# Performance work log

Hardware: AMD Instinct MI355X
Metric: run time of the kernel (lower is better)

The kernel has to match this reference:

```python
import jax, jax.numpy as jnp
import numpy as np

B, S, D, H = 64, 2048, 64, 128  # batch, seq_len, input_dim, rnn_hidden_dim


def setup_inputs() -> dict:
    key = jax.random.key(0)
    k = jax.random.split(key, 6)
    x = jax.random.normal(k[0], (B, S, D), dtype=jnp.float32)
    # LSTM params, keras gate order: i, f, g(candidate), o
    Wx = jax.random.normal(k[1], (D, 4 * H), dtype=jnp.float32) / np.sqrt(D)
    Wh = jax.random.normal(k[2], (H, 4 * H), dtype=jnp.float32) / np.sqrt(H)
    b = jnp.zeros((4 * H,), dtype=jnp.float32).at[H:2 * H].set(1.0)  # unit_forget_bias
    # Dense(1, sigmoid) head
    Wd = jax.random.normal(k[3], (H, 1), dtype=jnp.float32) / np.sqrt(H)
    bd = jnp.zeros((1,), dtype=jnp.float32)
    return {"x": x, "Wx": Wx, "Wh": Wh, "b": b, "Wd": Wd, "bd": bd}


def _lstm_seq(x, Wx, Wh, b):
    H_ = Wh.shape[0]
    # precompute input projections for all timesteps: [B,S,4H]
    xz = jnp.einsum('bsd,dg->bsg', x, Wx) + b

    def step(carry, xz_t):
        h, c = carry
        z = xz_t + h @ Wh  # [B,4H]
        i = jax.nn.sigmoid(z[:, :H_])
        f = jax.nn.sigmoid(z[:, H_:2 * H_])
        g = jnp.tanh(z[:, 2 * H_:3 * H_])
        o = jax.nn.sigmoid(z[:, 3 * H_:])
        c = f * c + i * g
        h = o * jnp.tanh(c)
        return (h, c), h

    h0 = jnp.zeros((x.shape[0], H_), dtype=x.dtype)
    c0 = jnp.zeros((x.shape[0], H_), dtype=x.dtype)
    _, hs = jax.lax.scan(step, (h0, c0), jnp.swapaxes(xz, 0, 1))  # hs: [S,B,H]
    return jnp.swapaxes(hs, 0, 1)  # [B,S,H]


def reference(x, Wx, Wh, b, Wd, bd):
    h = _lstm_seq(x, Wx, Wh, b)                 # [B,S,H]
    return jax.nn.sigmoid(h @ Wd + bd)          # [B,S,1]
```

## Files before the change

kernel.cpp:

```cpp
#include <hip/hip_runtime.h>

#define B_ 64
#define S_ 2048
#define D_ 64
#define H_ 128
#define G_ 512
#define CH 16

typedef float f32x4 __attribute__((ext_vector_type(4)));
typedef short bf16x8 __attribute__((ext_vector_type(8)));

#define MFMA16(a, b, c) __builtin_amdgcn_mfma_f32_16x16x32_bf16((a), (b), (c), 0, 0, 0)
#define RCPF(x) __builtin_amdgcn_rcpf(x)
#define LOG2E 1.442695041f

#if __has_builtin(__builtin_amdgcn_exp2f)
#define EXP2(x) __builtin_amdgcn_exp2f(x)
#else
#define EXP2(x) exp2f(x)
#endif

#define STEP_SYNC() do {                                  \
    asm volatile("s_waitcnt lgkmcnt(0)" ::: "memory");    \
    __builtin_amdgcn_s_barrier();                         \
    asm volatile("" ::: "memory");                        \
} while (0)

__device__ __forceinline__ short f2bf(float f) {
    unsigned u = __builtin_bit_cast(unsigned, f);
    return (short)((u + 0x7FFFu + ((u >> 16) & 1u)) >> 16);
}
__device__ __forceinline__ float bflo(unsigned u) { return __builtin_bit_cast(float, u << 16); }
__device__ __forceinline__ float bfhi(unsigned u) { return __builtin_bit_cast(float, u & 0xFFFF0000u); }
__device__ __forceinline__ float sigm_f(float x) { return RCPF(1.0f + EXP2(x * -LOG2E)); }

__launch_bounds__(512, 1)
__global__ void lstm_fused(const float* __restrict__ x, const float* __restrict__ Wx,
                           const float* __restrict__ Wh, const float* __restrict__ bias,
                           const float* __restrict__ Wd, const float* __restrict__ bd,
                           float* __restrict__ out) {
    const int tid = threadIdx.x;
    const int lane = tid & 63;
    const int wid = tid >> 6;
    const int l15 = lane & 15;
    const int l4 = lane >> 4;
    const int bb = blockIdx.x;

    __shared__ alignas(16) short hist[CH][H_];
    __shared__ alignas(16) short xbf[CH][72];
    __shared__ alignas(16) float xzc[CH][G_];

    ((unsigned*)hist)[tid] = 0u;
    ((unsigned*)hist)[tid + 512] = 0u;

    const int col0 = wid * 16 + l15;

    bf16x8 bh[4][4];
#pragma unroll
    for (int ct = 0; ct < 4; ++ct) {
        const float msc = (ct == 2) ? (-2.0f * LOG2E) : (-LOG2E);
        const int col = ct * H_ + col0;
#pragma unroll
        for (int kt = 0; kt < 4; ++kt) {
            bf16x8 v;
#pragma unroll
            for (int e = 0; e < 8; ++e)
                v[e] = f2bf(Wh[(kt * 32 + l4 * 8 + e) * G_ + col] * msc);
            bh[ct][kt] = v;
        }
    }
    bf16x8 bx[4][2];
#pragma unroll
    for (int ct = 0; ct < 4; ++ct) {
        const float msc = (ct == 2) ? (-2.0f * LOG2E) : (-LOG2E);
        const int col = ct * H_ + col0;
#pragma unroll
        for (int kt = 0; kt < 2; ++kt) {
            bf16x8 v;
#pragma unroll
            for (int e = 0; e < 8; ++e)
                v[e] = f2bf(Wx[(kt * 32 + l4 * 8 + e) * G_ + col] * msc);
            bx[ct][kt] = v;
        }
    }

    float bvr[4];
#pragma unroll
    for (int ct = 0; ct < 4; ++ct)
        bvr[ct] = bias[ct * H_ + col0] * ((ct == 2) ? (-2.0f * LOG2E) : (-LOG2E));
    const float wd0 = Wd[lane * 2 + 0];
    const float wd1 = Wd[lane * 2 + 1];
    const float bdv = bd[0];
    float c_reg = 0.0f;

    const float* xb = x + (size_t)bb * S_ * D_;
    float* ob = out + (size_t)bb * S_;

    float xp0 = xb[tid * 2 + 0];
    float xp1 = xb[tid * 2 + 1];

    f32x4 acc0 = {0.f, 0.f, 0.f, 0.f}, acc1 = acc0, acc2 = acc0, acc3 = acc0;

    for (int tc = 0; tc < S_; tc += CH) {
        xbf[tid >> 5][(tid & 31) * 2 + 0] = f2bf(xp0);
        xbf[tid >> 5][(tid & 31) * 2 + 1] = f2bf(xp1);
        __syncthreads();
        if (tc + CH < S_) {
            xp0 = xb[(tc + CH) * D_ + tid * 2 + 0];
            xp1 = xb[(tc + CH) * D_ + tid * 2 + 1];
        }
#pragma unroll
        for (int ct = 0; ct < 4; ++ct) {
            f32x4 cc = {bvr[ct], bvr[ct], bvr[ct], bvr[ct]};
#pragma unroll
            for (int kt = 0; kt < 2; ++kt) {
                const bf16x8 a = *reinterpret_cast<const bf16x8*>(&xbf[l15][kt * 32 + l4 * 8]);
                cc = MFMA16(a, bx[ct][kt], cc);
            }
#pragma unroll
            for (int r = 0; r < 4; ++r)
                xzc[l4 * 4 + r][col0 * 4 + ct] = cc[r];
        }
        if (tc > 0) {
#pragma unroll
            for (int s = 0; s < 2; ++s) {
                const int row = wid * 2 + s;
                const unsigned hp = *reinterpret_cast<const unsigned*>(&hist[row][lane * 2]);
                float p = bflo(hp) * wd0 + bfhi(hp) * wd1;
                p += __shfl_xor(p, 1);  p += __shfl_xor(p, 2);  p += __shfl_xor(p, 4);
                p += __shfl_xor(p, 8);  p += __shfl_xor(p, 16); p += __shfl_xor(p, 32);
                if (lane == 0) ob[tc - CH + row] = sigm_f(p + bdv);
            }
        }
        __syncthreads();

        f32x4 xzr[CH];
#pragma unroll
        for (int j = 0; j < CH; ++j)
            xzr[j] = *reinterpret_cast<const f32x4*>(&xzc[j][col0 * 4]);

#pragma unroll
        for (int tm = 0; tm < CH; ++tm) {
            const int prev = (tm + CH - 1) & (CH - 1);
            const short* hsrc = hist[prev];
            const bf16x8 a0 = *reinterpret_cast<const bf16x8*>(&hsrc[ 0 + l4 * 8]);
            const bf16x8 a1 = *reinterpret_cast<const bf16x8*>(&hsrc[32 + l4 * 8]);
            const bf16x8 a2 = *reinterpret_cast<const bf16x8*>(&hsrc[64 + l4 * 8]);
            const bf16x8 a3 = *reinterpret_cast<const bf16x8*>(&hsrc[96 + l4 * 8]);

            acc0[0] = xzr[tm][0];  acc1[0] = xzr[tm][1];
            acc2[0] = xzr[tm][2];  acc3[0] = xzr[tm][3];

            acc0 = MFMA16(a0, bh[0][0], acc0);
            acc1 = MFMA16(a0, bh[1][0], acc1);
            acc2 = MFMA16(a0, bh[2][0], acc2);
            acc3 = MFMA16(a0, bh[3][0], acc3);
            acc0 = MFMA16(a1, bh[0][1], acc0);
            acc1 = MFMA16(a1, bh[1][1], acc1);
            acc2 = MFMA16(a1, bh[2][1], acc2);
            acc3 = MFMA16(a1, bh[3][1], acc3);
            acc0 = MFMA16(a2, bh[0][2], acc0);
            acc1 = MFMA16(a2, bh[1][2], acc1);
            acc2 = MFMA16(a2, bh[2][2], acc2);
            acc3 = MFMA16(a2, bh[3][2], acc3);
            acc0 = MFMA16(a3, bh[0][3], acc0);
            acc1 = MFMA16(a3, bh[1][3], acc1);
            acc2 = MFMA16(a3, bh[2][3], acc2);
            acc3 = MFMA16(a3, bh[3][3], acc3);

            const float iv = RCPF(1.0f + EXP2(acc0[0]));
            const float fv = RCPF(1.0f + EXP2(acc1[0]));
            const float gv = __builtin_fmaf(2.0f, RCPF(1.0f + EXP2(acc2[0])), -1.0f);
            const float ov = RCPF(1.0f + EXP2(acc3[0]));

            c_reg = __builtin_fmaf(fv, c_reg, iv * gv);
            const float th = __builtin_fmaf(
                2.0f, RCPF(1.0f + EXP2(c_reg * (-2.0f * LOG2E))), -1.0f);
            const float hv = ov * th;

            if (lane < 16) hist[tm][col0] = f2bf(hv);
            STEP_SYNC();
        }
    }

#pragma unroll
    for (int s = 0; s < 2; ++s) {
        const int row = wid * 2 + s;
        const unsigned hp = *reinterpret_cast<const unsigned*>(&hist[row][lane * 2]);
        float p = bflo(hp) * wd0 + bfhi(hp) * wd1;
        p += __shfl_xor(p, 1);  p += __shfl_xor(p, 2);  p += __shfl_xor(p, 4);
        p += __shfl_xor(p, 8);  p += __shfl_xor(p, 16); p += __shfl_xor(p, 32);
        if (lane == 0) ob[S_ - CH + row] = sigm_f(p + bdv);
    }
}

extern "C" void kernel_launch(void* const* d_in, const int* in_sizes, int n_in,
                              void* d_out, int out_size, void* d_ws, size_t ws_size,
                              hipStream_t stream) {
    const float* x  = (const float*)d_in[0];
    const float* Wx = (const float*)d_in[1];
    const float* Wh = (const float*)d_in[2];
    const float* b  = (const float*)d_in[3];
    const float* Wd = (const float*)d_in[4];
    const float* bd = (const float*)d_in[5];
    float* out = (float*)d_out;

    lstm_fused<<<B_, 512, 0, stream>>>(x, Wx, Wh, b, Wd, bd, out);
}
```

Baseline: 884.1 us.

## Switch recurrent MFMA to fp16 and split K-chain into two accumulators

```diff
diff --git a/kernel.cpp b/kernel.cpp
--- a/kernel.cpp
+++ b/kernel.cpp
@@ -8,9 +8,10 @@
 #define CH 16
 
 typedef float f32x4 __attribute__((ext_vector_type(4)));
-typedef short bf16x8 __attribute__((ext_vector_type(8)));
-
-#define MFMA16(a, b, c) __builtin_amdgcn_mfma_f32_16x16x32_bf16((a), (b), (c), 0, 0, 0)
+typedef _Float16 f16x8 __attribute__((ext_vector_type(8)));
+typedef _Float16 f16x2 __attribute__((ext_vector_type(2)));
+
+#define MFMA16H(a, b, c) __builtin_amdgcn_mfma_f32_16x16x32_f16((a), (b), (c), 0, 0, 0)
 #define RCPF(x) __builtin_amdgcn_rcpf(x)
 #define LOG2E 1.442695041f
 
@@ -26,12 +27,6 @@
     asm volatile("" ::: "memory");                        \
 } while (0)
 
-__device__ __forceinline__ short f2bf(float f) {
-    unsigned u = __builtin_bit_cast(unsigned, f);
-    return (short)((u + 0x7FFFu + ((u >> 16) & 1u)) >> 16);
-}
-__device__ __forceinline__ float bflo(unsigned u) { return __builtin_bit_cast(float, u << 16); }
-__device__ __forceinline__ float bfhi(unsigned u) { return __builtin_bit_cast(float, u & 0xFFFF0000u); }
 __device__ __forceinline__ float sigm_f(float x) { return RCPF(1.0f + EXP2(x * -LOG2E)); }
 
 __launch_bounds__(512, 1)
@@ -46,8 +41,8 @@
     const int l4 = lane >> 4;
     const int bb = blockIdx.x;
 
-    __shared__ alignas(16) short hist[CH][H_];
-    __shared__ alignas(16) short xbf[CH][72];
+    __shared__ alignas(16) _Float16 hist[CH][H_];
+    __shared__ alignas(16) _Float16 xbf[CH][72];
     __shared__ alignas(16) float xzc[CH][G_];
 
     ((unsigned*)hist)[tid] = 0u;
@@ -55,31 +50,31 @@
 
     const int col0 = wid * 16 + l15;
 
-    bf16x8 bh[4][4];
+    f16x8 bh[4][4];
 #pragma unroll
     for (int ct = 0; ct < 4; ++ct) {
         const float msc = (ct == 2) ? (-2.0f * LOG2E) : (-LOG2E);
         const int col = ct * H_ + col0;
 #pragma unroll
         for (int kt = 0; kt < 4; ++kt) {
-            bf16x8 v;
+            f16x8 v;
 #pragma unroll
             for (int e = 0; e < 8; ++e)
-                v[e] = f2bf(Wh[(kt * 32 + l4 * 8 + e) * G_ + col] * msc);
+                v[e] = (_Float16)(Wh[(kt * 32 + l4 * 8 + e) * G_ + col] * msc);
             bh[ct][kt] = v;
         }
     }
-    bf16x8 bx[4][2];
+    f16x8 bx[4][2];
 #pragma unroll
     for (int ct = 0; ct < 4; ++ct) {
         const float msc = (ct == 2) ? (-2.0f * LOG2E) : (-LOG2E);
         const int col = ct * H_ + col0;
 #pragma unroll
         for (int kt = 0; kt < 2; ++kt) {
-            bf16x8 v;
+            f16x8 v;
 #pragma unroll
             for (int e = 0; e < 8; ++e)
-                v[e] = f2bf(Wx[(kt * 32 + l4 * 8 + e) * G_ + col] * msc);
+                v[e] = (_Float16)(Wx[(kt * 32 + l4 * 8 + e) * G_ + col] * msc);
             bx[ct][kt] = v;
         }
     }
@@ -99,11 +94,12 @@
     float xp0 = xb[tid * 2 + 0];
     float xp1 = xb[tid * 2 + 1];
 
-    f32x4 acc0 = {0.f, 0.f, 0.f, 0.f}, acc1 = acc0, acc2 = acc0, acc3 = acc0;
+    f32x4 p0a = {0.f, 0.f, 0.f, 0.f}, p0b = p0a, p1a = p0a, p1b = p0a;
+    f32x4 p2a = p0a, p2b = p0a, p3a = p0a, p3b = p0a;
 
     for (int tc = 0; tc < S_; tc += CH) {
-        xbf[tid >> 5][(tid & 31) * 2 + 0] = f2bf(xp0);
-        xbf[tid >> 5][(tid & 31) * 2 + 1] = f2bf(xp1);
+        xbf[tid >> 5][(tid & 31) * 2 + 0] = (_Float16)xp0;
+        xbf[tid >> 5][(tid & 31) * 2 + 1] = (_Float16)xp1;
         __syncthreads();
         if (tc + CH < S_) {
             xp0 = xb[(tc + CH) * D_ + tid * 2 + 0];
@@ -114,8 +110,8 @@
             f32x4 cc = {bvr[ct], bvr[ct], bvr[ct], bvr[ct]};
 #pragma unroll
             for (int kt = 0; kt < 2; ++kt) {
-                const bf16x8 a = *reinterpret_cast<const bf16x8*>(&xbf[l15][kt * 32 + l4 * 8]);
-                cc = MFMA16(a, bx[ct][kt], cc);
+                const f16x8 a = *reinterpret_cast<const f16x8*>(&xbf[l15][kt * 32 + l4 * 8]);
+                cc = MFMA16H(a, bx[ct][kt], cc);
             }
 #pragma unroll
             for (int r = 0; r < 4; ++r)
@@ -125,8 +121,8 @@
 #pragma unroll
             for (int s = 0; s < 2; ++s) {
                 const int row = wid * 2 + s;
-                const unsigned hp = *reinterpret_cast<const unsigned*>(&hist[row][lane * 2]);
-                float p = bflo(hp) * wd0 + bfhi(hp) * wd1;
+                const f16x2 hp = *reinterpret_cast<const f16x2*>(&hist[row][lane * 2]);
+                float p = (float)hp[0] * wd0 + (float)hp[1] * wd1;
                 p += __shfl_xor(p, 1);  p += __shfl_xor(p, 2);  p += __shfl_xor(p, 4);
                 p += __shfl_xor(p, 8);  p += __shfl_xor(p, 16); p += __shfl_xor(p, 32);
                 if (lane == 0) ob[tc - CH + row] = sigm_f(p + bdv);
@@ -142,43 +138,40 @@
 #pragma unroll
         for (int tm = 0; tm < CH; ++tm) {
             const int prev = (tm + CH - 1) & (CH - 1);
-            const short* hsrc = hist[prev];
-            const bf16x8 a0 = *reinterpret_cast<const bf16x8*>(&hsrc[ 0 + l4 * 8]);
-            const bf16x8 a1 = *reinterpret_cast<const bf16x8*>(&hsrc[32 + l4 * 8]);
-            const bf16x8 a2 = *reinterpret_cast<const bf16x8*>(&hsrc[64 + l4 * 8]);
-            const bf16x8 a3 = *reinterpret_cast<const bf16x8*>(&hsrc[96 + l4 * 8]);
-
-            acc0[0] = xzr[tm][0];  acc1[0] = xzr[tm][1];
-            acc2[0] = xzr[tm][2];  acc3[0] = xzr[tm][3];
-
-            acc0 = MFMA16(a0, bh[0][0], acc0);
-            acc1 = MFMA16(a0, bh[1][0], acc1);
-            acc2 = MFMA16(a0, bh[2][0], acc2);
-            acc3 = MFMA16(a0, bh[3][0], acc3);
-            acc0 = MFMA16(a1, bh[0][1], acc0);
-            acc1 = MFMA16(a1, bh[1][1], acc1);
-            acc2 = MFMA16(a1, bh[2][1], acc2);
-            acc3 = MFMA16(a1, bh[3][1], acc3);
-            acc0 = MFMA16(a2, bh[0][2], acc0);
-            acc1 = MFMA16(a2, bh[1][2], acc1);
-            acc2 = MFMA16(a2, bh[2][2], acc2);
-            acc3 = MFMA16(a2, bh[3][2], acc3);
-            acc0 = MFMA16(a3, bh[0][3], acc0);
-            acc1 = MFMA16(a3, bh[1][3], acc1);
-            acc2 = MFMA16(a3, bh[2][3], acc2);
-            acc3 = MFMA16(a3, bh[3][3], acc3);
-
-            const float iv = RCPF(1.0f + EXP2(acc0[0]));
-            const float fv = RCPF(1.0f + EXP2(acc1[0]));
-            const float gv = __builtin_fmaf(2.0f, RCPF(1.0f + EXP2(acc2[0])), -1.0f);
-            const float ov = RCPF(1.0f + EXP2(acc3[0]));
+            const _Float16* hsrc = hist[prev];
+            const f16x8 a0 = *reinterpret_cast<const f16x8*>(&hsrc[ 0 + l4 * 8]);
+            const f16x8 a1 = *reinterpret_cast<const f16x8*>(&hsrc[32 + l4 * 8]);
+            const f16x8 a2 = *reinterpret_cast<const f16x8*>(&hsrc[64 + l4 * 8]);
+            const f16x8 a3 = *reinterpret_cast<const f16x8*>(&hsrc[96 + l4 * 8]);
+
+            p0a[0] = xzr[tm][0];  p1a[0] = xzr[tm][1];
+            p2a[0] = xzr[tm][2];  p3a[0] = xzr[tm][3];
+            p0b[0] = 0.f;  p1b[0] = 0.f;  p2b[0] = 0.f;  p3b[0] = 0.f;
+
+            p0a = MFMA16H(a0, bh[0][0], p0a);  p0b = MFMA16H(a2, bh[0][2], p0b);
+            p1a = MFMA16H(a0, bh[1][0], p1a);  p1b = MFMA16H(a2, bh[1][2], p1b);
+            p2a = MFMA16H(a0, bh[2][0], p2a);  p2b = MFMA16H(a2, bh[2][2], p2b);
+            p3a = MFMA16H(a0, bh[3][0], p3a);  p3b = MFMA16H(a2, bh[3][2], p3b);
+            p0a = MFMA16H(a1, bh[0][1], p0a);  p0b = MFMA16H(a3, bh[0][3], p0b);
+            p1a = MFMA16H(a1, bh[1][1], p1a);  p1b = MFMA16H(a3, bh[1][3], p1b);
+            p2a = MFMA16H(a1, bh[2][1], p2a);  p2b = MFMA16H(a3, bh[2][3], p2b);
+            p3a = MFMA16H(a1, bh[3][1], p3a);  p3b = MFMA16H(a3, bh[3][3], p3b);
+
+            const float zi = p0a[0] + p0b[0];
+            const float zf = p1a[0] + p1b[0];
+            const float zg = p2a[0] + p2b[0];
+            const float zo = p3a[0] + p3b[0];
+            const float iv = RCPF(1.0f + EXP2(zi));
+            const float fv = RCPF(1.0f + EXP2(zf));
+            const float gv = __builtin_fmaf(2.0f, RCPF(1.0f + EXP2(zg)), -1.0f);
+            const float ov = RCPF(1.0f + EXP2(zo));
 
             c_reg = __builtin_fmaf(fv, c_reg, iv * gv);
             const float th = __builtin_fmaf(
                 2.0f, RCPF(1.0f + EXP2(c_reg * (-2.0f * LOG2E))), -1.0f);
             const float hv = ov * th;
 
-            if (lane < 16) hist[tm][col0] = f2bf(hv);
+            if (lane < 16) hist[tm][col0] = (_Float16)hv;
             STEP_SYNC();
         }
     }
@@ -186,8 +179,8 @@
 #pragma unroll
     for (int s = 0; s < 2; ++s) {
         const int row = wid * 2 + s;
-        const unsigned hp = *reinterpret_cast<const unsigned*>(&hist[row][lane * 2]);
-        float p = bflo(hp) * wd0 + bfhi(hp) * wd1;
+        const f16x2 hp = *reinterpret_cast<const f16x2*>(&hist[row][lane * 2]);
+        float p = (float)hp[0] * wd0 + (float)hp[1] * wd1;
         p += __shfl_xor(p, 1);  p += __shfl_xor(p, 2);  p += __shfl_xor(p, 4);
         p += __shfl_xor(p, 8);  p += __shfl_xor(p, 16); p += __shfl_xor(p, 32);
         if (lane == 0) ob[S_ - CH + row] = sigm_f(p + bdv);
```

Measured after the change: 964.6 us. 1.09x slower.
